# Performance work log

Measured on AMD Instinct MI355X. Metric: run time of the kernel, lower is better.

## Reference

```python
import jax, jax.numpy as jnp
import numpy as np

N_NODES = 100000
N_REL = 8
N_EDGES = 80000
IN_F, HID, OUT = 128, 32, 2
N_GRAPHS = 64


def setup_inputs() -> dict:
    key = jax.random.key(0)
    ks = jax.random.split(key, 12)
    x = jax.random.normal(ks[0], (N_NODES, IN_F), dtype=jnp.float32)
    src = jax.random.randint(ks[1], (N_REL, N_EDGES), 0, N_NODES, dtype=jnp.int32)
    dst = jax.random.randint(ks[2], (N_REL, N_EDGES), 0, N_NODES, dtype=jnp.int32)
    graph_ids = jax.random.randint(ks[3], (N_NODES,), 0, N_GRAPHS, dtype=jnp.int32)
    W1 = jax.random.normal(ks[4], (N_REL, IN_F, HID), dtype=jnp.float32) / np.sqrt(IN_F)
    b1 = jnp.zeros((N_REL, HID), dtype=jnp.float32)
    W2 = jax.random.normal(ks[5], (N_REL, HID, HID), dtype=jnp.float32) / np.sqrt(HID)
    b2 = jnp.zeros((N_REL, HID), dtype=jnp.float32)
    Wc = jax.random.normal(ks[6], (HID, OUT), dtype=jnp.float32) / np.sqrt(HID)
    bc = jnp.zeros((OUT,), dtype=jnp.float32)
    return {"x": x, "src": src, "dst": dst, "graph_ids": graph_ids,
            "num_graphs": N_GRAPHS, "W1": W1, "b1": b1, "W2": W2, "b2": b2,
            "Wc": Wc, "bc": bc}


def _hetero_conv(h, src, dst, W, b, n_nodes):
    """HeteroGraphConv(sum) of per-relation GraphConv(norm='both')."""
    n_rel = W.shape[0]
    out = jnp.zeros((n_nodes, W.shape[2]), dtype=h.dtype)
    ones_e = jnp.ones((src.shape[1],), dtype=h.dtype)
    for r in range(n_rel):  # small fixed relation set
        s, d = src[r], dst[r]
        # symmetric normalization with degree clamped to >= 1 (DGL behavior)
        deg_out = jnp.maximum(jax.ops.segment_sum(ones_e, s, num_segments=n_nodes), 1.0)
        deg_in = jnp.maximum(jax.ops.segment_sum(ones_e, d, num_segments=n_nodes), 1.0)
        hn = h * jax.lax.rsqrt(deg_out)[:, None]      # [N, F_in]
        hw = hn @ W[r]                                # project first (F_in >= F_out)
        agg = jax.ops.segment_sum(hw[s], d, num_segments=n_nodes)  # scatter-sum to dst
        out = out + agg * jax.lax.rsqrt(deg_in)[:, None] + b[r]
    return out


def reference(x, src, dst, graph_ids, num_graphs, W1, b1, W2, b2, Wc, bc):
    n = x.shape[0]
    h = jax.nn.relu(_hetero_conv(x, src, dst, W1, b1, n))
    h = _hetero_conv(h, src, dst, W2, b2, n)
    # per-graph mean pooling over nodes
    sums = jax.ops.segment_sum(h, graph_ids, num_segments=num_graphs)
    cnts = jnp.maximum(jax.ops.segment_sum(jnp.ones((n,), h.dtype), graph_ids,
                                           num_segments=num_graphs), 1.0)
    pooled = sums / cnts[:, None]
    return pooled @ Wc + bc
```

## Files before the change

### kernel.cpp

```cpp
#include <hip/hip_runtime.h>


#define N_NODES 100000
#define N_REL   8
#define N_EDGES 80000
#define IN_F    128
#define HID     32
#define N_GRAPHS 64
#define NCAT    (N_REL * HID)
#define N_KEYS  (N_NODES * N_REL)
#define TOT_E   (N_REL * N_EDGES)

constexpr int TILE = 256;
constexpr int KC   = 32;

typedef __attribute__((ext_vector_type(8))) short bf16x8;
typedef __attribute__((ext_vector_type(4))) float f32x4;

__device__ __forceinline__ ushort f2bf(float v) {
  unsigned u = __builtin_bit_cast(unsigned, v);
  u = (u + 0x7fffu + ((u >> 16) & 1u)) >> 16;
  return (ushort)u;
}
__device__ __forceinline__ float bf2f(ushort h) {
  unsigned u = ((unsigned)h) << 16;
  return __builtin_bit_cast(float, u);
}

__global__ __launch_bounds__(256) void deg_hist_kernel(const int* __restrict__ src, const int* __restrict__ dst,
                                                       int* __restrict__ dego, int* __restrict__ cnt) {
  int i = blockIdx.x * 256 + threadIdx.x;
  int s = src[i], d = dst[i];
  int r = i / N_EDGES;
  atomicAdd(&dego[r * N_NODES + s], 1);
  atomicAdd(&cnt[d * N_REL + r], 1);
}

__global__ __launch_bounds__(256) void rsqrt_kernel(float* __restrict__ p, int count) {
  int i = blockIdx.x * 256 + threadIdx.x;
  if (i < count) {
    int d = ((const int*)p)[i];
    p[i] = rsqrtf((float)(d < 1 ? 1 : d));
  }
}

__global__ __launch_bounds__(256) void prep_w_kernel(const float* __restrict__ W1, const float* __restrict__ W2,
                                                     const float* __restrict__ Wc,
                                                     ushort* __restrict__ Wt1, ushort* __restrict__ Vt) {
  int i = blockIdx.x * 256 + threadIdx.x;
  if (i < NCAT * IN_F) {
    int n = i >> 7, k = i & 127;
    int r = n >> 5, j = n & 31;
    Wt1[i] = f2bf(W1[r * (IN_F * HID) + k * HID + j]);
  } else {
    int q = i - NCAT * IN_F;
    if (q < 16 * HID) {
      int n = q >> 5, k = q & 31;
      int r = n >> 1, c = n & 1;
      float s = 0.f;
#pragma unroll
      for (int j = 0; j < HID; j++) s += W2[r * (HID * HID) + k * HID + j] * Wc[j * 2 + c];
      Vt[q] = f2bf(s);
    }
  }
}

__global__ __launch_bounds__(256) void scan1_kernel(const int* __restrict__ in, int* __restrict__ out,
                                                    int* __restrict__ partial, int n) {
  __shared__ int ts[256];
  int b0 = blockIdx.x * 1024;
  int t = threadIdx.x;
  int v[4]; int s = 0;
#pragma unroll
  for (int k = 0; k < 4; k++) {
    int idx = b0 + t * 4 + k;
    v[k] = s;
    s += (idx < n) ? in[idx] : 0;
  }
  ts[t] = s;
  __syncthreads();
  for (int off = 1; off < 256; off <<= 1) {
    int xv = (t >= off) ? ts[t - off] : 0;
    __syncthreads();
    ts[t] += xv;
    __syncthreads();
  }
  int texcl = (t == 0) ? 0 : ts[t - 1];
#pragma unroll
  for (int k = 0; k < 4; k++) {
    int idx = b0 + t * 4 + k;
    if (idx < n) out[idx] = texcl + v[k];
  }
  if (t == 255) partial[blockIdx.x] = ts[255];
}

__global__ __launch_bounds__(256) void scan2_kernel(int* __restrict__ partial, int nb) {
  __shared__ int ts[256];
  int t = threadIdx.x;
  int v[4]; int s = 0;
#pragma unroll
  for (int k = 0; k < 4; k++) {
    int idx = t * 4 + k;
    v[k] = s;
    s += (idx < nb) ? partial[idx] : 0;
  }
  ts[t] = s;
  __syncthreads();
  for (int off = 1; off < 256; off <<= 1) {
    int xv = (t >= off) ? ts[t - off] : 0;
    __syncthreads();
    ts[t] += xv;
    __syncthreads();
  }
  int texcl = (t == 0) ? 0 : ts[t - 1];
#pragma unroll
  for (int k = 0; k < 4; k++) {
    int idx = t * 4 + k;
    if (idx < nb) partial[idx] = texcl + v[k];
  }
}

__global__ __launch_bounds__(256) void scan3_kernel(int* __restrict__ out, const int* __restrict__ partial, int n) {
  int i = blockIdx.x * 256 + threadIdx.x;
  if (i < n) out[i] += partial[i >> 10];
  if (i == 0) out[n] = TOT_E;
}

__global__ __launch_bounds__(256) void fill_kernel(const int* __restrict__ src, const int* __restrict__ dst,
                                                   const int* __restrict__ rp, int* __restrict__ fillc,
                                                   const int* __restrict__ cnt,
                                                   int* __restrict__ ecol1, int* __restrict__ ecol2,
                                                   float* __restrict__ ew) {
  int i = blockIdx.x * 256 + threadIdx.x;
  int d = dst[i];
  int s = src[i];
  int r = i / N_EDGES;
  int key = d * N_REL + r;
  int c = cnt[key];
  int pos = atomicAdd(&fillc[key], 1);
  int t = rp[key] + pos;
  ecol1[t] = s * NCAT + r * HID;
  ecol2[t] = s * 16 + r * 2;
  ew[t] = rsqrtf((float)(c < 1 ? 1 : c));
}

__global__ __launch_bounds__(256, 4) void gemm1_staged(const float* __restrict__ A, const ushort* __restrict__ Bt,
                                                       const float* __restrict__ rs_o, ushort* __restrict__ Y, int M) {
  __shared__ ushort smem[17408];
  int wave = __builtin_amdgcn_readfirstlane(threadIdx.x >> 6);
  int lane = threadIdx.x & 63;
  int t = threadIdx.x;
  int m0 = (blockIdx.x * 4 + wave) * 16;
  int me = (m0 <= M - 16) ? m0 : (M - 16);
  int row = lane & 15, quad = lane >> 4;

  bf16x8 af[4];
#pragma unroll
  for (int kq = 0; kq < 4; kq++) {
    const float* ap = &A[(size_t)(me + row) * IN_F + kq * 32 + quad * 8];
    float4 a0 = *(const float4*)ap;
    float4 a1 = *(const float4*)(ap + 4);
    bf16x8 a;
    a[0] = (short)f2bf(a0.x); a[1] = (short)f2bf(a0.y); a[2] = (short)f2bf(a0.z); a[3] = (short)f2bf(a0.w);
    a[4] = (short)f2bf(a1.x); a[5] = (short)f2bf(a1.y); a[6] = (short)f2bf(a1.z); a[7] = (short)f2bf(a1.w);
    af[kq] = a;
  }

  f32x4 acc[16];
#pragma unroll
  for (int nt = 0; nt < 16; nt++) acc[nt] = (f32x4){0.f, 0.f, 0.f, 0.f};

  for (int p = 0; p < 2; p++) {
    __syncthreads();
    const ushort* bsrc = Bt + (size_t)p * (128 * IN_F);
#pragma unroll
    for (int i = 0; i < 8; i++) {
      int c = t + i * 256;
      int rr2 = c >> 4, cc = c & 15;
      uint4 v = *(const uint4*)&bsrc[rr2 * IN_F + cc * 8];
      *(uint4*)&smem[rr2 * 136 + cc * 8] = v;
    }
    __syncthreads();
#pragma unroll
    for (int kq = 0; kq < 4; kq++) {
#pragma unroll
      for (int nt2 = 0; nt2 < 8; nt2++) {
        bf16x8 b = *(const bf16x8*)&smem[(nt2 * 16 + row) * 136 + kq * 32 + quad * 8];
        acc[p * 8 + nt2] = __builtin_amdgcn_mfma_f32_16x16x32_bf16(af[kq], b, acc[p * 8 + nt2], 0, 0, 0);
      }
    }
  }
  __syncthreads();

  float4 sc[N_REL];
#pragma unroll
  for (int r = 0; r < N_REL; r++)
    sc[r] = *(const float4*)&rs_o[(size_t)r * N_NODES + me + quad * 4];
  ushort* myt = &smem[wave * 4160];
#pragma unroll
  for (int nt = 0; nt < 16; nt++) {
    const float* s4 = (const float*)&sc[nt >> 1];
#pragma unroll
    for (int i = 0; i < 4; i++)
      myt[(quad * 4 + i) * 260 + nt * 16 + row] = f2bf(acc[nt][i] * s4[i]);
  }
  if (m0 <= M - 16) {
    ushort* ybase = &Y[(size_t)m0 * NCAT];
#pragma unroll
    for (int k = 0; k < 8; k++) {
      int g = k * 512 + lane * 8;
      int r2 = g >> 8, c2 = g & 255;
      const ushort* sp = &myt[r2 * 260 + c2];
      uint4 v;
      v.x = *(const uint*)(sp + 0);
      v.y = *(const uint*)(sp + 2);
      v.z = *(const uint*)(sp + 4);
      v.w = *(const uint*)(sp + 6);
      *(uint4*)&ybase[g] = v;
    }
  }
}

__global__ __launch_bounds__(256) void gemm2_mfma(const ushort* __restrict__ H, const ushort* __restrict__ Vt,
                                                  const float* __restrict__ rs_o, float* __restrict__ Ys2, int M) {
  int wave = __builtin_amdgcn_readfirstlane(threadIdx.x >> 6);
  int lane = threadIdx.x & 63;
  int m0 = (blockIdx.x * 4 + wave) * 16;
  if (m0 >= M) return;
  int row = lane & 15, quad = lane >> 4;
  f32x4 acc = (f32x4){0.f, 0.f, 0.f, 0.f};
  bf16x8 a = *(const bf16x8*)&H[(size_t)(m0 + row) * HID + quad * 8];
  bf16x8 b = *(const bf16x8*)&Vt[row * HID + quad * 8];
  acc = __builtin_amdgcn_mfma_f32_16x16x32_bf16(a, b, acc, 0, 0, 0);
  int r = row >> 1;
#pragma unroll
  for (int i = 0; i < 4; i++) {
    int m = m0 + quad * 4 + i;
    Ys2[(size_t)m * 16 + row] = acc[i] * rs_o[(size_t)r * N_NODES + m];
  }
}

__global__ __launch_bounds__(256) void gather1_kernel(const ushort* __restrict__ Ys, const int* __restrict__ ecol1,
                                                      const float* __restrict__ ew, const int* __restrict__ rp,
                                                      const float* __restrict__ b1, ushort* __restrict__ H) {
  int wave = __builtin_amdgcn_readfirstlane(threadIdx.x >> 6);
  int lane = threadIdx.x & 63;
  int d = blockIdx.x * 4 + wave;
  if (d >= N_NODES) return;
  int j = lane & 31, half = lane >> 5;
  int base = rp[d * N_REL], endp = rp[d * N_REL + N_REL];
  float sum = 0.f;
  for (int t = base + half; t < endp; t += 2) {
    int off = ecol1[t];
    float w = ew[t];
    sum += w * bf2f(Ys[(size_t)off + j]);
  }
  sum += __shfl_down(sum, 32);
  if (half == 0) {
    float sb = 0.f;
#pragma unroll
    for (int q = 0; q < N_REL; q++) sb += b1[q * HID + j];
    H[(size_t)d * HID + j] = f2bf(fmaxf(sum + sb, 0.f));
  }
}

__global__ __launch_bounds__(256) void gather2_pool_kernel(const float* __restrict__ Ys2,
                                                           const int* __restrict__ ecol2,
                                                           const float* __restrict__ ew, const int* __restrict__ rp,
                                                           const int* __restrict__ gid,
                                                           float* __restrict__ gpool, float* __restrict__ gcnt) {
  __shared__ float lp[N_GRAPHS * 2];
  __shared__ float lc[N_GRAPHS];
  int t = threadIdx.x;
  if (t < N_GRAPHS * 2) lp[t] = 0.f;
  if (t < N_GRAPHS) lc[t] = 0.f;
  __syncthreads();
  for (int n = blockIdx.x * 256 + t; n < N_NODES; n += gridDim.x * 256) {
    int base = rp[n * N_REL], endp = rp[n * N_REL + N_REL];
    float z0 = 0.f, z1 = 0.f;
    for (int s = base; s < endp; s++) {
      float w = ew[s];
      float2 y = *(const float2*)&Ys2[ecol2[s]];
      z0 += w * y.x;
      z1 += w * y.y;
    }
    int g = gid[n];
    atomicAdd(&lp[g * 2 + 0], z0);
    atomicAdd(&lp[g * 2 + 1], z1);
    atomicAdd(&lc[g], 1.f);
  }
  __syncthreads();
  if (t < N_GRAPHS * 2) atomicAdd(&gpool[t], lp[t]);
  if (t < N_GRAPHS) atomicAdd(&gcnt[t], lc[t]);
}

__global__ void final_kernel(const float* __restrict__ gpool, const float* __restrict__ gcnt,
                             const float* __restrict__ b2, const float* __restrict__ Wc,
                             const float* __restrict__ bc, float* __restrict__ out) {
  int g = threadIdx.x;
  if (g >= N_GRAPHS) return;
  float c0 = 0.f, c1 = 0.f;
#pragma unroll
  for (int k = 0; k < HID; k++) {
    float sb = 0.f;
#pragma unroll
    for (int r = 0; r < N_REL; r++) sb += b2[r * HID + k];
    c0 += sb * Wc[k * 2 + 0];
    c1 += sb * Wc[k * 2 + 1];
  }
  float cntv = gcnt[g];
  if (cntv > 0.f) {
    out[g * 2 + 0] = gpool[g * 2 + 0] / cntv + c0 + bc[0];
    out[g * 2 + 1] = gpool[g * 2 + 1] / cntv + c1 + bc[1];
  } else {
    out[g * 2 + 0] = bc[0];
    out[g * 2 + 1] = bc[1];
  }
}

__global__ __launch_bounds__(256) void deg_kernel(const int* __restrict__ src, const int* __restrict__ dst,
                                                  int* __restrict__ dego, int* __restrict__ degi, int n_rel) {
  int i = blockIdx.x * 256 + threadIdx.x;
  if (i < n_rel * N_EDGES) {
    int r = i / N_EDGES;
    atomicAdd(&dego[r * N_NODES + src[i]], 1);
    atomicAdd(&degi[r * N_NODES + dst[i]], 1);
  }
}

__global__ __launch_bounds__(256) void proj1_kernel(const float* __restrict__ x, const float* __restrict__ W1r0,
                                                    const float* __restrict__ rs_o, float* __restrict__ hw,
                                                    int n0, int n1, int hw_nodes) {
  int rr = blockIdx.y;
  int nb = n0 + blockIdx.x * TILE;
  int t = threadIdx.x;
  __shared__ float xs[TILE][KC + 4];
  const float* __restrict__ Wr = W1r0 + (size_t)rr * (IN_F * HID);
  float acc[HID];
#pragma unroll
  for (int j = 0; j < HID; j++) acc[j] = 0.f;
  for (int kc = 0; kc < IN_F; kc += KC) {
    __syncthreads();
#pragma unroll
    for (int i = 0; i < (TILE * KC / 4) / 256; i++) {
      int q = t + i * 256;
      int nn = q >> 3, k4 = q & 7;
      int n = nb + nn;
      float4 v = make_float4(0.f, 0.f, 0.f, 0.f);
      if (n < n1) v = *(const float4*)&x[(size_t)n * IN_F + kc + k4 * 4];
      *(float4*)&xs[nn][k4 * 4] = v;
    }
    __syncthreads();
#pragma unroll
    for (int k4 = 0; k4 < KC / 4; k4++) {
      float4 xv = *(const float4*)&xs[t][k4 * 4];
      const float* wk = &Wr[(kc + k4 * 4) * HID];
#pragma unroll
      for (int j = 0; j < HID; j++) acc[j] += xv.x * wk[j];
#pragma unroll
      for (int j = 0; j < HID; j++) acc[j] += xv.y * wk[HID + j];
#pragma unroll
      for (int j = 0; j < HID; j++) acc[j] += xv.z * wk[2 * HID + j];
#pragma unroll
      for (int j = 0; j < HID; j++) acc[j] += xv.w * wk[3 * HID + j];
    }
  }
  int n = nb + t;
  if (n < n1) {
    float s = rs_o[(size_t)rr * N_NODES + n];
    float* o = &hw[((size_t)rr * hw_nodes + (n - n0)) * HID];
#pragma unroll
    for (int j4 = 0; j4 < HID / 4; j4++) {
      float4 v = make_float4(acc[j4 * 4] * s, acc[j4 * 4 + 1] * s, acc[j4 * 4 + 2] * s, acc[j4 * 4 + 3] * s);
      *(float4*)&o[j4 * 4] = v;
    }
  }
}

__global__ __launch_bounds__(256) void proj2_kernel(const float* __restrict__ acc1, const float* __restrict__ b1,
                                                    const float* __restrict__ W2r0, const float* __restrict__ rs_o,
                                                    float* __restrict__ hw, int n0, int n1, int hw_nodes) {
  int n = n0 + blockIdx.x * 256 + threadIdx.x;
  if (n >= n1) return;
  int rr = blockIdx.y;
  float h1[HID];
#pragma unroll
  for (int j4 = 0; j4 < HID / 4; j4++) {
    float4 v = *(const float4*)&acc1[(size_t)n * HID + j4 * 4];
    h1[j4 * 4 + 0] = v.x; h1[j4 * 4 + 1] = v.y; h1[j4 * 4 + 2] = v.z; h1[j4 * 4 + 3] = v.w;
  }
#pragma unroll
  for (int j = 0; j < HID; j++) {
    float sb = 0.f;
#pragma unroll
    for (int q = 0; q < N_REL; q++) sb += b1[q * HID + j];
    h1[j] = fmaxf(h1[j] + sb, 0.f);
  }
  const float* __restrict__ Wr = W2r0 + (size_t)rr * (HID * HID);
  float acc[HID];
#pragma unroll
  for (int j = 0; j < HID; j++) acc[j] = 0.f;
#pragma unroll
  for (int k = 0; k < HID; k++) {
    float hv = h1[k];
#pragma unroll
    for (int j = 0; j < HID; j++) acc[j] += hv * Wr[k * HID + j];
  }
  float s = rs_o[(size_t)rr * N_NODES + n];
  float* o = &hw[((size_t)rr * hw_nodes + (n - n0)) * HID];
#pragma unroll
  for (int j4 = 0; j4 < HID / 4; j4++) {
    float4 v = make_float4(acc[j4 * 4] * s, acc[j4 * 4 + 1] * s, acc[j4 * 4 + 2] * s, acc[j4 * 4 + 3] * s);
    *(float4*)&o[j4 * 4] = v;
  }
}

__global__ __launch_bounds__(256) void scatter_kernel(const float* __restrict__ hw, const int* __restrict__ src,
                                                      const int* __restrict__ dst, const float* __restrict__ rs_i,
                                                      float* __restrict__ acc, int nr, int n0, int n1, int hw_nodes) {
  long i = (long)blockIdx.x * 256 + threadIdx.x;
  long total = (long)nr * N_EDGES * HID;
  if (i >= total) return;
  int j = (int)(i & (HID - 1));
  long e = i >> 5;
  int rr = (int)(e / N_EDGES);
  int ee = (int)(e - (long)rr * N_EDGES);
  int s = src[rr * N_EDGES + ee];
  if (s < n0 || s >= n1) return;
  int d = dst[rr * N_EDGES + ee];
  float v = hw[((size_t)rr * hw_nodes + (s - n0)) * HID + j] * rs_i[(size_t)rr * N_NODES + d];
  atomicAdd(&acc[(size_t)d * HID + j], v);
}

__global__ __launch_bounds__(256) void pool_kernel(const float* __restrict__ acc2, const float* __restrict__ b2,
                                                   const int* __restrict__ gid, float* __restrict__ gpool,
                                                   float* __restrict__ gcnt) {
  __shared__ float lp[N_GRAPHS * HID];
  __shared__ float lc[N_GRAPHS];
  int t = threadIdx.x;
  for (int i = t; i < N_GRAPHS * HID; i += 256) lp[i] = 0.f;
  if (t < N_GRAPHS) lc[t] = 0.f;
  __syncthreads();
  int j = t & (HID - 1);
  int grp = t >> 5;
  float sb = 0.f;
#pragma unroll
  for (int q = 0; q < N_REL; q++) sb += b2[q * HID + j];
  for (int n = blockIdx.x * 8 + grp; n < N_NODES; n += gridDim.x * 8) {
    int g = gid[n];
    float v = acc2[(size_t)n * HID + j] + sb;
    atomicAdd(&lp[g * HID + j], v);
    if (j == 0) atomicAdd(&lc[g], 1.f);
  }
  __syncthreads();
  for (int i = t; i < N_GRAPHS * HID; i += 256) atomicAdd(&gpool[i], lp[i]);
  if (t < N_GRAPHS) atomicAdd(&gcnt[t], lc[t]);
}

__global__ void final3_kernel(const float* __restrict__ gpool, const float* __restrict__ gcnt,
                              const float* __restrict__ Wc, const float* __restrict__ bc,
                              float* __restrict__ out) {
  int g = threadIdx.x;
  if (g >= N_GRAPHS) return;
  float inv = 1.f / fmaxf(gcnt[g], 1.f);
  float o0 = bc[0], o1 = bc[1];
#pragma unroll
  for (int k = 0; k < HID; k++) {
    float p = gpool[g * HID + k] * inv;
    o0 += p * Wc[k * 2 + 0];
    o1 += p * Wc[k * 2 + 1];
  }
  out[g * 2 + 0] = o0;
  out[g * 2 + 1] = o1;
}

extern "C" void kernel_launch(void* const* d_in, const int* in_sizes, int n_in,
                              void* d_out, int out_size, void* d_ws, size_t ws_size,
                              hipStream_t stream) {
  const float* x  = (const float*)d_in[0];
  const int* src  = (const int*)d_in[1];
  const int* dst  = (const int*)d_in[2];
  const int* gid  = (const int*)d_in[3];
  const float* W1 = (const float*)d_in[5];
  const float* b1 = (const float*)d_in[6];
  const float* W2 = (const float*)d_in[7];
  const float* b2 = (const float*)d_in[8];
  const float* Wc = (const float*)d_in[9];
  const float* bc = (const float*)d_in[10];
  float* out = (float*)d_out;

  float* ws = (float*)d_ws;
  const size_t NF = (size_t)N_NODES * HID;
  const size_t RN = (size_t)N_REL * N_NODES;
  const size_t POOLF = N_GRAPHS * HID + N_GRAPHS;
  size_t wsf = ws_size / 4;

  const size_t T1_NEED = 22500000;

  if (wsf >= T1_NEED) {
    float* gpool = ws;
    float* gcnt  = gpool + N_GRAPHS * 2;
    float* rs_o  = gcnt + N_GRAPHS;
    int*   cnt   = (int*)(rs_o + RN);
    int*   fillc = cnt + N_KEYS;
    int*   rp    = fillc + N_KEYS;
    int*   part  = rp + N_KEYS + 8;
    int*   ecol1 = part + 1024;
    int*   ecol2 = ecol1 + TOT_E;
    float* ew    = (float*)(ecol2 + TOT_E);
    float* Ys2   = ew + TOT_E;
    ushort* Ys   = (ushort*)(Ys2 + (size_t)N_NODES * 16);
    ushort* Hbf  = Ys + (size_t)N_NODES * NCAT;
    ushort* Wt1  = Hbf + (size_t)N_NODES * HID;
    ushort* Vt   = Wt1 + NCAT * IN_F;

    size_t zbytes = (N_GRAPHS * 3 + RN + 2 * (size_t)N_KEYS) * 4;
    hipMemsetAsync(ws, 0, zbytes, stream);

    deg_hist_kernel<<<TOT_E / 256, 256, 0, stream>>>(src, dst, (int*)rs_o, cnt);
    rsqrt_kernel<<<(int)((RN + 255) / 256), 256, 0, stream>>>(rs_o, (int)RN);
    prep_w_kernel<<<(NCAT * IN_F + 16 * HID + 255) / 256, 256, 0, stream>>>(W1, W2, Wc, Wt1, Vt);

    int sblocks = (N_KEYS + 1023) / 1024;
    scan1_kernel<<<sblocks, 256, 0, stream>>>(cnt, rp, part, N_KEYS);
    scan2_kernel<<<1, 256, 0, stream>>>(part, sblocks);
    scan3_kernel<<<(N_KEYS + 255) / 256, 256, 0, stream>>>(rp, part, N_KEYS);
    fill_kernel<<<TOT_E / 256, 256, 0, stream>>>(src, dst, rp, fillc, cnt, ecol1, ecol2, ew);

    int gblocks = (N_NODES / 16 + 3) / 4;
    int nblocks = (N_NODES + 3) / 4;
    gemm1_staged<<<gblocks, 256, 0, stream>>>(x, Wt1, rs_o, Ys, N_NODES);
    gather1_kernel<<<nblocks, 256, 0, stream>>>(Ys, ecol1, ew, rp, b1, Hbf);
    gemm2_mfma<<<gblocks, 256, 0, stream>>>(Hbf, Vt, rs_o, Ys2, N_NODES);
    gather2_pool_kernel<<<416, 256, 0, stream>>>(Ys2, ecol2, ew, rp, gid, gpool, gcnt);
    final_kernel<<<1, 64, 0, stream>>>(gpool, gcnt, b2, Wc, bc, out);
  } else {
    float* acc1  = ws;
    float* acc2  = acc1 + NF;
    float* gpool = acc2 + NF;
    float* gcnt  = gpool + N_GRAPHS * HID;
    float* rsb   = ws + (2 * NF + POOLF);
    size_t zf = 2 * NF + POOLF;
    float* rs_o = rsb;
    float* rs_i = rsb + N_NODES;
    float* hw = rsb + 2 * N_NODES;
    size_t fixed3 = zf + 2 * N_NODES;
    size_t avail = (wsf > fixed3) ? (wsf - fixed3) : 0;
    long chunk = (long)(avail / HID) & ~255L;
    if (chunk < 256) chunk = 256;
    if (chunk > N_NODES) chunk = N_NODES;

    size_t zb = zf * 4; if (zb > ws_size) zb = ws_size;
    hipMemsetAsync(d_ws, 0, zb, stream);

    for (int layer = 0; layer < 2; layer++) {
      for (int r = 0; r < N_REL; r++) {
        hipMemsetAsync(rs_o, 0, 2 * N_NODES * 4, stream);
        deg_kernel<<<(N_EDGES + 255) / 256, 256, 0, stream>>>(src + (size_t)r * N_EDGES, dst + (size_t)r * N_EDGES,
                                                              (int*)rs_o, (int*)rs_i, 1);
        rsqrt_kernel<<<(2 * N_NODES + 255) / 256, 256, 0, stream>>>(rs_o, 2 * N_NODES);
        for (long n0 = 0; n0 < N_NODES; n0 += chunk) {
          long n1 = n0 + chunk; if (n1 > N_NODES) n1 = N_NODES;
          int tiles = (int)((n1 - n0 + TILE - 1) / TILE);
          if (layer == 0)
            proj1_kernel<<<dim3(tiles, 1), 256, 0, stream>>>(x, W1 + (size_t)r * IN_F * HID, rs_o, hw,
                                                             (int)n0, (int)n1, (int)chunk);
          else
            proj2_kernel<<<dim3(tiles, 1), 256, 0, stream>>>(acc1, b1, W2 + (size_t)r * HID * HID, rs_o, hw,
                                                             (int)n0, (int)n1, (int)chunk);
          long tot = (long)N_EDGES * HID;
          scatter_kernel<<<(int)((tot + 255) / 256), 256, 0, stream>>>(hw, src + (size_t)r * N_EDGES,
                                                                       dst + (size_t)r * N_EDGES, rs_i,
                                                                       layer == 0 ? acc1 : acc2,
                                                                       1, (int)n0, (int)n1, (int)chunk);
        }
      }
    }
    pool_kernel<<<256, 256, 0, stream>>>(acc2, b2, gid, gpool, gcnt);
    final3_kernel<<<1, 64, 0, stream>>>(gpool, gcnt, Wc, bc, out);
  }
}
```

Baseline: 308.2 us.

## Fuse degree histogram into GEMM1 and fold source norm into edge weights

Merges the degree-histogram atomics and the first projection GEMM into one launch with interleaved block roles, so the two independent pieces of work overlap on the GPU. The per-source rsqrt(deg_out) scaling moves out of both GEMM epilogues and into a per-edge weight computed in fill_kernel. Edge column indices and weights are packed into one int4 record so the gathers issue a single load per edge. The costs are a wider per-edge record (16 bytes versus 12), a runtime role branch inside the GEMM kernel, and fewer launches overall.

```diff
diff --git a/kernel.cpp b/kernel.cpp
--- a/kernel.cpp
+++ b/kernel.cpp
@@ -10,6 +10,8 @@
 #define NCAT    (N_REL * HID)
 #define N_KEYS  (N_NODES * N_REL)
 #define TOT_E   (N_REL * N_EDGES)
+#define DEG_BLOCKS  (TOT_E / 256)
+#define GEMM_BLOCKS ((N_NODES / 16 + 3) / 4)
 
 constexpr int TILE = 256;
 constexpr int KC   = 32;
@@ -25,15 +27,6 @@
 __device__ __forceinline__ float bf2f(ushort h) {
   unsigned u = ((unsigned)h) << 16;
   return __builtin_bit_cast(float, u);
-}
-
-__global__ __launch_bounds__(256) void deg_hist_kernel(const int* __restrict__ src, const int* __restrict__ dst,
-                                                       int* __restrict__ dego, int* __restrict__ cnt) {
-  int i = blockIdx.x * 256 + threadIdx.x;
-  int s = src[i], d = dst[i];
-  int r = i / N_EDGES;
-  atomicAdd(&dego[r * N_NODES + s], 1);
-  atomicAdd(&cnt[d * N_REL + r], 1);
 }
 
 __global__ __launch_bounds__(256) void rsqrt_kernel(float* __restrict__ p, int count) {
@@ -65,92 +58,29 @@
   }
 }
 
-__global__ __launch_bounds__(256) void scan1_kernel(const int* __restrict__ in, int* __restrict__ out,
-                                                    int* __restrict__ partial, int n) {
-  __shared__ int ts[256];
-  int b0 = blockIdx.x * 1024;
-  int t = threadIdx.x;
-  int v[4]; int s = 0;
-#pragma unroll
-  for (int k = 0; k < 4; k++) {
-    int idx = b0 + t * 4 + k;
-    v[k] = s;
-    s += (idx < n) ? in[idx] : 0;
-  }
-  ts[t] = s;
-  __syncthreads();
-  for (int off = 1; off < 256; off <<= 1) {
-    int xv = (t >= off) ? ts[t - off] : 0;
-    __syncthreads();
-    ts[t] += xv;
-    __syncthreads();
-  }
-  int texcl = (t == 0) ? 0 : ts[t - 1];
-#pragma unroll
-  for (int k = 0; k < 4; k++) {
-    int idx = b0 + t * 4 + k;
-    if (idx < n) out[idx] = texcl + v[k];
-  }
-  if (t == 255) partial[blockIdx.x] = ts[255];
-}
-
-__global__ __launch_bounds__(256) void scan2_kernel(int* __restrict__ partial, int nb) {
-  __shared__ int ts[256];
-  int t = threadIdx.x;
-  int v[4]; int s = 0;
-#pragma unroll
-  for (int k = 0; k < 4; k++) {
-    int idx = t * 4 + k;
-    v[k] = s;
-    s += (idx < nb) ? partial[idx] : 0;
-  }
-  ts[t] = s;
-  __syncthreads();
-  for (int off = 1; off < 256; off <<= 1) {
-    int xv = (t >= off) ? ts[t - off] : 0;
-    __syncthreads();
-    ts[t] += xv;
-    __syncthreads();
-  }
-  int texcl = (t == 0) ? 0 : ts[t - 1];
-#pragma unroll
-  for (int k = 0; k < 4; k++) {
-    int idx = t * 4 + k;
-    if (idx < nb) partial[idx] = texcl + v[k];
-  }
-}
-
-__global__ __launch_bounds__(256) void scan3_kernel(int* __restrict__ out, const int* __restrict__ partial, int n) {
-  int i = blockIdx.x * 256 + threadIdx.x;
-  if (i < n) out[i] += partial[i >> 10];
-  if (i == 0) out[n] = TOT_E;
-}
-
-__global__ __launch_bounds__(256) void fill_kernel(const int* __restrict__ src, const int* __restrict__ dst,
-                                                   const int* __restrict__ rp, int* __restrict__ fillc,
-                                                   const int* __restrict__ cnt,
-                                                   int* __restrict__ ecol1, int* __restrict__ ecol2,
-                                                   float* __restrict__ ew) {
-  int i = blockIdx.x * 256 + threadIdx.x;
-  int d = dst[i];
-  int s = src[i];
-  int r = i / N_EDGES;
-  int key = d * N_REL + r;
-  int c = cnt[key];
-  int pos = atomicAdd(&fillc[key], 1);
-  int t = rp[key] + pos;
-  ecol1[t] = s * NCAT + r * HID;
-  ecol2[t] = s * 16 + r * 2;
-  ew[t] = rsqrtf((float)(c < 1 ? 1 : c));
-}
-
-__global__ __launch_bounds__(256, 4) void gemm1_staged(const float* __restrict__ A, const ushort* __restrict__ Bt,
-                                                       const float* __restrict__ rs_o, ushort* __restrict__ Y, int M) {
+__global__ __launch_bounds__(256, 4) void fused_deg_gemm1(const int* __restrict__ src, const int* __restrict__ dst,
+                                                          int* __restrict__ dego, int* __restrict__ cnt,
+                                                          const float* __restrict__ A, const ushort* __restrict__ Bt,
+                                                          ushort* __restrict__ Y, int M) {
   __shared__ ushort smem[17408];
+  int bid = blockIdx.x;
+  int isg, rid;
+  if (bid < 2 * GEMM_BLOCKS) { isg = !(bid & 1); rid = bid >> 1; }
+  else { isg = 0; rid = GEMM_BLOCKS + (bid - 2 * GEMM_BLOCKS); }
+
+  if (!isg) {
+    int i = rid * 256 + (int)threadIdx.x;
+    int s = src[i], d = dst[i];
+    int r = i / N_EDGES;
+    atomicAdd(&dego[r * N_NODES + s], 1);
+    atomicAdd(&cnt[d * N_REL + r], 1);
+    return;
+  }
+
   int wave = __builtin_amdgcn_readfirstlane(threadIdx.x >> 6);
   int lane = threadIdx.x & 63;
   int t = threadIdx.x;
-  int m0 = (blockIdx.x * 4 + wave) * 16;
+  int m0 = (rid * 4 + wave) * 16;
   int me = (m0 <= M - 16) ? m0 : (M - 16);
   int row = lane & 15, quad = lane >> 4;
 
@@ -192,17 +122,12 @@
   }
   __syncthreads();
 
-  float4 sc[N_REL];
-#pragma unroll
-  for (int r = 0; r < N_REL; r++)
-    sc[r] = *(const float4*)&rs_o[(size_t)r * N_NODES + me + quad * 4];
   ushort* myt = &smem[wave * 4160];
 #pragma unroll
   for (int nt = 0; nt < 16; nt++) {
-    const float* s4 = (const float*)&sc[nt >> 1];
 #pragma unroll
     for (int i = 0; i < 4; i++)
-      myt[(quad * 4 + i) * 260 + nt * 16 + row] = f2bf(acc[nt][i] * s4[i]);
+      myt[(quad * 4 + i) * 260 + nt * 16 + row] = f2bf(acc[nt][i]);
   }
   if (m0 <= M - 16) {
     ushort* ybase = &Y[(size_t)m0 * NCAT];
@@ -221,8 +146,90 @@
   }
 }
 
+__global__ __launch_bounds__(256) void scan1_kernel(const int* __restrict__ in, int* __restrict__ out,
+                                                    int* __restrict__ partial, int n) {
+  __shared__ int ts[256];
+  int b0 = blockIdx.x * 1024;
+  int t = threadIdx.x;
+  int v[4]; int s = 0;
+#pragma unroll
+  for (int k = 0; k < 4; k++) {
+    int idx = b0 + t * 4 + k;
+    v[k] = s;
+    s += (idx < n) ? in[idx] : 0;
+  }
+  ts[t] = s;
+  __syncthreads();
+  for (int off = 1; off < 256; off <<= 1) {
+    int xv = (t >= off) ? ts[t - off] : 0;
+    __syncthreads();
+    ts[t] += xv;
+    __syncthreads();
+  }
+  int texcl = (t == 0) ? 0 : ts[t - 1];
+#pragma unroll
+  for (int k = 0; k < 4; k++) {
+    int idx = b0 + t * 4 + k;
+    if (idx < n) out[idx] = texcl + v[k];
+  }
+  if (t == 255) partial[blockIdx.x] = ts[255];
+}
+
+__global__ __launch_bounds__(256) void scan2_kernel(int* __restrict__ partial, int nb) {
+  __shared__ int ts[256];
+  int t = threadIdx.x;
+  int v[4]; int s = 0;
+#pragma unroll
+  for (int k = 0; k < 4; k++) {
+    int idx = t * 4 + k;
+    v[k] = s;
+    s += (idx < nb) ? partial[idx] : 0;
+  }
+  ts[t] = s;
+  __syncthreads();
+  for (int off = 1; off < 256; off <<= 1) {
+    int xv = (t >= off) ? ts[t - off] : 0;
+    __syncthreads();
+    ts[t] += xv;
+    __syncthreads();
+  }
+  int texcl = (t == 0) ? 0 : ts[t - 1];
+#pragma unroll
+  for (int k = 0; k < 4; k++) {
+    int idx = t * 4 + k;
+    if (idx < nb) partial[idx] = texcl + v[k];
+  }
+}
+
+__global__ __launch_bounds__(256) void scan3_kernel(int* __restrict__ out, const int* __restrict__ partial, int n) {
+  int i = blockIdx.x * 256 + threadIdx.x;
+  if (i < n) out[i] += partial[i >> 10];
+  if (i == 0) out[n] = TOT_E;
+}
+
+__global__ __launch_bounds__(256) void fill_kernel(const int* __restrict__ src, const int* __restrict__ dst,
+                                                   const int* __restrict__ rp, int* __restrict__ fillc,
+                                                   const int* __restrict__ cnt, const float* __restrict__ rs_o,
+                                                   int4* __restrict__ edata) {
+  int i = blockIdx.x * 256 + threadIdx.x;
+  int d = dst[i];
+  int s = src[i];
+  int r = i / N_EDGES;
+  int key = d * N_REL + r;
+  int c = cnt[key];
+  int pos = atomicAdd(&fillc[key], 1);
+  int t = rp[key] + pos;
+  float w = rs_o[r * N_NODES + s] * rsqrtf((float)(c < 1 ? 1 : c));
+  int4 e;
+  e.x = s * NCAT + r * HID;
+  e.y = s * 16 + r * 2;
+  e.z = __builtin_bit_cast(int, w);
+  e.w = 0;
+  edata[t] = e;
+}
+
 __global__ __launch_bounds__(256) void gemm2_mfma(const ushort* __restrict__ H, const ushort* __restrict__ Vt,
-                                                  const float* __restrict__ rs_o, float* __restrict__ Ys2, int M) {
+                                                  float* __restrict__ Ys2, int M) {
   int wave = __builtin_amdgcn_readfirstlane(threadIdx.x >> 6);
   int lane = threadIdx.x & 63;
   int m0 = (blockIdx.x * 4 + wave) * 16;
@@ -232,16 +239,15 @@
   bf16x8 a = *(const bf16x8*)&H[(size_t)(m0 + row) * HID + quad * 8];
   bf16x8 b = *(const bf16x8*)&Vt[row * HID + quad * 8];
   acc = __builtin_amdgcn_mfma_f32_16x16x32_bf16(a, b, acc, 0, 0, 0);
-  int r = row >> 1;
 #pragma unroll
   for (int i = 0; i < 4; i++) {
     int m = m0 + quad * 4 + i;
-    Ys2[(size_t)m * 16 + row] = acc[i] * rs_o[(size_t)r * N_NODES + m];
-  }
-}
-
-__global__ __launch_bounds__(256) void gather1_kernel(const ushort* __restrict__ Ys, const int* __restrict__ ecol1,
-                                                      const float* __restrict__ ew, const int* __restrict__ rp,
+    Ys2[(size_t)m * 16 + row] = acc[i];
+  }
+}
+
+__global__ __launch_bounds__(256) void gather1_kernel(const ushort* __restrict__ Ys, const int4* __restrict__ edata,
+                                                      const int* __restrict__ rp,
                                                       const float* __restrict__ b1, ushort* __restrict__ H) {
   int wave = __builtin_amdgcn_readfirstlane(threadIdx.x >> 6);
   int lane = threadIdx.x & 63;
@@ -251,9 +257,9 @@
   int base = rp[d * N_REL], endp = rp[d * N_REL + N_REL];
   float sum = 0.f;
   for (int t = base + half; t < endp; t += 2) {
-    int off = ecol1[t];
-    float w = ew[t];
-    sum += w * bf2f(Ys[(size_t)off + j]);
+    int4 e = edata[t];
+    float w = __builtin_bit_cast(float, e.z);
+    sum += w * bf2f(Ys[(size_t)e.x + j]);
   }
   sum += __shfl_down(sum, 32);
   if (half == 0) {
@@ -265,8 +271,8 @@
 }
 
 __global__ __launch_bounds__(256) void gather2_pool_kernel(const float* __restrict__ Ys2,
-                                                           const int* __restrict__ ecol2,
-                                                           const float* __restrict__ ew, const int* __restrict__ rp,
+                                                           const int4* __restrict__ edata,
+                                                           const int* __restrict__ rp,
                                                            const int* __restrict__ gid,
                                                            float* __restrict__ gpool, float* __restrict__ gcnt) {
   __shared__ float lp[N_GRAPHS * 2];
@@ -279,8 +285,9 @@
     int base = rp[n * N_REL], endp = rp[n * N_REL + N_REL];
     float z0 = 0.f, z1 = 0.f;
     for (int s = base; s < endp; s++) {
-      float w = ew[s];
-      float2 y = *(const float2*)&Ys2[ecol2[s]];
+      int4 e = edata[s];
+      float w = __builtin_bit_cast(float, e.z);
+      float2 y = *(const float2*)&Ys2[e.y];
       z0 += w * y.x;
       z1 += w * y.y;
     }
@@ -505,10 +512,8 @@
     int*   fillc = cnt + N_KEYS;
     int*   rp    = fillc + N_KEYS;
     int*   part  = rp + N_KEYS + 8;
-    int*   ecol1 = part + 1024;
-    int*   ecol2 = ecol1 + TOT_E;
-    float* ew    = (float*)(ecol2 + TOT_E);
-    float* Ys2   = ew + TOT_E;
+    int4*  edata = (int4*)(part + 1024);
+    float* Ys2   = (float*)(edata + TOT_E);
     ushort* Ys   = (ushort*)(Ys2 + (size_t)N_NODES * 16);
     ushort* Hbf  = Ys + (size_t)N_NODES * NCAT;
     ushort* Wt1  = Hbf + (size_t)N_NODES * HID;
@@ -517,22 +522,22 @@
     size_t zbytes = (N_GRAPHS * 3 + RN + 2 * (size_t)N_KEYS) * 4;
     hipMemsetAsync(ws, 0, zbytes, stream);
 
-    deg_hist_kernel<<<TOT_E / 256, 256, 0, stream>>>(src, dst, (int*)rs_o, cnt);
+    prep_w_kernel<<<(NCAT * IN_F + 16 * HID + 255) / 256, 256, 0, stream>>>(W1, W2, Wc, Wt1, Vt);
+    fused_deg_gemm1<<<DEG_BLOCKS + GEMM_BLOCKS, 256, 0, stream>>>(src, dst, (int*)rs_o, cnt,
+                                                                  x, Wt1, Ys, N_NODES);
     rsqrt_kernel<<<(int)((RN + 255) / 256), 256, 0, stream>>>(rs_o, (int)RN);
-    prep_w_kernel<<<(NCAT * IN_F + 16 * HID + 255) / 256, 256, 0, stream>>>(W1, W2, Wc, Wt1, Vt);
 
     int sblocks = (N_KEYS + 1023) / 1024;
     scan1_kernel<<<sblocks, 256, 0, stream>>>(cnt, rp, part, N_KEYS);
     scan2_kernel<<<1, 256, 0, stream>>>(part, sblocks);
     scan3_kernel<<<(N_KEYS + 255) / 256, 256, 0, stream>>>(rp, part, N_KEYS);
-    fill_kernel<<<TOT_E / 256, 256, 0, stream>>>(src, dst, rp, fillc, cnt, ecol1, ecol2, ew);
-
-    int gblocks = (N_NODES / 16 + 3) / 4;
+    fill_kernel<<<TOT_E / 256, 256, 0, stream>>>(src, dst, rp, fillc, cnt, rs_o, edata);
+
+    int gblocks = GEMM_BLOCKS;
     int nblocks = (N_NODES + 3) / 4;
-    gemm1_staged<<<gblocks, 256, 0, stream>>>(x, Wt1, rs_o, Ys, N_NODES);
-    gather1_kernel<<<nblocks, 256, 0, stream>>>(Ys, ecol1, ew, rp, b1, Hbf);
-    gemm2_mfma<<<gblocks, 256, 0, stream>>>(Hbf, Vt, rs_o, Ys2, N_NODES);
-    gather2_pool_kernel<<<416, 256, 0, stream>>>(Ys2, ecol2, ew, rp, gid, gpool, gcnt);
+    gather1_kernel<<<nblocks, 256, 0, stream>>>(Ys, edata, rp, b1, Hbf);
+    gemm2_mfma<<<gblocks, 256, 0, stream>>>(Hbf, Vt, Ys2, N_NODES);
+    gather2_pool_kernel<<<416, 256, 0, stream>>>(Ys2, edata, rp, gid, gpool, gcnt);
     final_kernel<<<1, 64, 0, stream>>>(gpool, gcnt, b2, Wc, bc, out);
   } else {
     float* acc1  = ws;
```

Measured after the change: 280.3 us. -9.1%, faster.
